# Performance work log

Hardware: AMD Instinct MI355X
Metric: run time of the kernel (lower is better)

The kernel has to match this reference:

```python
import jax, jax.numpy as jnp
import numpy as np

TEMP = 8.0      # config.router_temp
TOP_K = 2       # config.moe_top_k
EPS = 1e-8
LN_EPS = 1e-5


def _layer_norm_noaffine(x):
    # nn.LayerNorm(input_dim, elementwise_affine=False)
    mu = jnp.mean(x, axis=-1, keepdims=True)
    var = jnp.var(x, axis=-1, keepdims=True)
    return (x - mu) / jnp.sqrt(var + LN_EPS)


def _unit_norm(x):
    # x / x.norm(dim=-1).clamp(min=EPS)
    n = jnp.linalg.norm(x, axis=-1, keepdims=True)
    return x / jnp.maximum(n, EPS)


def setup_inputs() -> dict:
    key = jax.random.key(0)
    k1, k2 = jax.random.split(key)
    x = jax.random.normal(k1, (4, 4096, 2048), dtype=jnp.float32)
    prototypes = jax.random.normal(k2, (64, 2048), dtype=jnp.float32)
    return {"x": x, "prototypes": prototypes}


def reference(x, prototypes):
    # input_norm_fn = 'norm_d', proto_norm_fn = 'unit'
    xn = _layer_norm_noaffine(x)          # [b, s, d]
    pn = _unit_norm(prototypes)           # [e, d]
    logits = jnp.einsum('bsd,ed->bse', xn, pn) / TEMP   # [b, s, e]
    probs = jax.nn.softmax(logits, axis=-1)
    top_w, top_i = jax.lax.top_k(probs, TOP_K)          # [b, s, k]
    top_w = top_w / jnp.sum(top_w, axis=-1, keepdims=True)
    return top_w, top_i
```

## Files before the change

kernel.cpp:

```cpp
#include <hip/hip_runtime.h>
#include <math.h>

constexpr int kD        = 2048;
constexpr int kE        = 64;
constexpr int kWaves    = 8;
constexpr int kBlockTok = 64;
constexpr int kKpw      = kD / kWaves;
constexpr int kBK       = 16;
constexpr int kTiles    = kKpw / kBK;
constexpr int kXsStride = 20;
constexpr int kBufStride = kE + 2;

__global__ __launch_bounds__(256) void proto_prep(const float* __restrict__ p,
                                                  float* __restrict__ ws) {
  const int e   = blockIdx.x;
  const int tid = threadIdx.x;
  const float4* row = (const float4*)(p + (size_t)e * kD);
  float s = 0.f, q = 0.f;
  for (int j = tid; j < kD / 4; j += 256) {
    float4 v = row[j];
    s += (v.x + v.y) + (v.z + v.w);
    q = fmaf(v.x, v.x, fmaf(v.y, v.y, fmaf(v.z, v.z, fmaf(v.w, v.w, q))));
  }
  #pragma unroll
  for (int off = 32; off >= 1; off >>= 1) {
    s += __shfl_xor(s, off, 64);
    q += __shfl_xor(q, off, 64);
  }
  __shared__ float as[4], aq[4];
  if ((tid & 63) == 0) { as[tid >> 6] = s; aq[tid >> 6] = q; }
  __syncthreads();
  if (tid == 0) {
    float S = (as[0] + as[1]) + (as[2] + as[3]);
    float Q = (aq[0] + aq[1]) + (aq[2] + aq[3]);
    float n = fmaxf(sqrtf(Q), 1e-8f);
    ws[e]      = S;
    ws[kE + e] = 1.f / n;
  }
}

__global__ __launch_bounds__(512, 2) void router_main(
    const float* __restrict__ x, const float* __restrict__ p,
    const float* __restrict__ ws, float* __restrict__ out_w,
    float* __restrict__ out_i) {
  __shared__ float xs_all[kWaves][kBlockTok][kXsStride];
  __shared__ float buf[kBlockTok * kBufStride];
  __shared__ float sSx[kWaves][kBlockTok];
  __shared__ float sSxx[kWaves][kBlockTok];

  const int w    = threadIdx.x >> 6;
  const int lane = threadIdx.x & 63;
  const int tt   = lane & 7;
  const int te   = lane >> 3;
  const int tok0 = blockIdx.x * kBlockTok;

  const float* xw = x + (size_t)tok0 * kD + w * kKpw;
  const float* pw = p + w * kKpw;
  float* xs = &xs_all[w][0][0];

  float acc[8][8];
  #pragma unroll
  for (int i = 0; i < 8; ++i)
    #pragma unroll
    for (int j = 0; j < 8; ++j) acc[i][j] = 0.f;
  float sx = 0.f, sxx = 0.f;

  for (int kt = 0; kt < kTiles; ++kt) {
    const float* gsrc = xw + kt * kBK;
    #pragma unroll
    for (int jj = 0; jj < 4; ++jj) {
      int f = lane + 64 * jj;
      int row = f >> 2;
      int c4  = f & 3;
      float4 v = *(const float4*)(gsrc + (size_t)row * kD + c4 * 4);
      *(float4*)(xs + row * kXsStride + c4 * 4) = v;
    }
    #pragma unroll
    for (int j = 0; j < 4; ++j) {
      float4 v = *(const float4*)(xs + lane * kXsStride + j * 4);
      sx += (v.x + v.y) + (v.z + v.w);
      sxx = fmaf(v.x, v.x, fmaf(v.y, v.y, fmaf(v.z, v.z, fmaf(v.w, v.w, sxx))));
    }
    const float* pt = pw + kt * kBK;
    #pragma unroll
    for (int k4 = 0; k4 < 4; ++k4) {
      float4 pf[8];
      #pragma unroll
      for (int j = 0; j < 8; ++j)
        pf[j] = *(const float4*)(pt + (size_t)(te + 8 * j) * kD + k4 * 4);
      float4 xf[8];
      #pragma unroll
      for (int i = 0; i < 8; ++i)
        xf[i] = *(const float4*)(xs + (tt + 8 * i) * kXsStride + k4 * 4);
      #pragma unroll
      for (int i = 0; i < 8; ++i)
        #pragma unroll
        for (int j = 0; j < 8; ++j) {
          acc[i][j] = fmaf(xf[i].x, pf[j].x, acc[i][j]);
          acc[i][j] = fmaf(xf[i].y, pf[j].y, acc[i][j]);
          acc[i][j] = fmaf(xf[i].z, pf[j].z, acc[i][j]);
          acc[i][j] = fmaf(xf[i].w, pf[j].w, acc[i][j]);
        }
    }
  }

  sSx[w][lane]  = sx;
  sSxx[w][lane] = sxx;

  for (int ph = 0; ph < kWaves; ++ph) {
    __syncthreads();
    if (w == ph) {
      #pragma unroll
      for (int i = 0; i < 8; ++i)
        #pragma unroll
        for (int j = 0; j < 8; ++j) {
          float* dst = &buf[(tt + 8 * i) * kBufStride + (te + 8 * j)];
          if (ph == 0) *dst = acc[i][j];
          else         *dst += acc[i][j];
        }
    }
  }
  __syncthreads();

  const float Se  = ws[lane];
  const float inv = ws[kE + lane];
  #pragma unroll
  for (int tl = 0; tl < 8; ++tl) {
    int t = w * 8 + tl;
    float Sx = 0.f, Sq = 0.f;
    #pragma unroll
    for (int q = 0; q < kWaves; ++q) { Sx += sSx[q][t]; Sq += sSxx[q][t]; }
    float mu   = Sx * (1.f / kD);
    float var  = Sq * (1.f / kD) - mu * mu;
    float rstd = rsqrtf(var + 1e-5f);
    float Dv   = buf[t * kBufStride + lane];
    float logit = (Dv - mu * Se) * rstd * inv * 0.125f;

    float v1 = logit; int i1 = lane;
    #pragma unroll
    for (int off = 32; off >= 1; off >>= 1) {
      float ov = __shfl_xor(v1, off, 64);
      int   oi = __shfl_xor(i1, off, 64);
      if (ov > v1 || (ov == v1 && oi < i1)) { v1 = ov; i1 = oi; }
    }
    float ml = (lane == i1) ? -3.402823466e38f : logit;
    float v2 = ml; int i2 = lane;
    #pragma unroll
    for (int off = 32; off >= 1; off >>= 1) {
      float ov = __shfl_xor(v2, off, 64);
      int   oi = __shfl_xor(i2, off, 64);
      if (ov > v2 || (ov == v2 && oi < i2)) { v2 = ov; i2 = oi; }
    }
    if (lane == 0) {
      int tg = tok0 + t;
      float er = expf(v2 - v1);
      float r  = 1.f / (1.f + er);
      out_w[2 * tg]     = r;
      out_w[2 * tg + 1] = er * r;
      out_i[2 * tg]     = (float)i1;
      out_i[2 * tg + 1] = (float)i2;
    }
  }
}

extern "C" void kernel_launch(void* const* d_in, const int* in_sizes, int n_in,
                              void* d_out, int out_size, void* d_ws, size_t ws_size,
                              hipStream_t stream) {
  const float* x = (const float*)d_in[0];
  const float* p = (const float*)d_in[1];
  float* ws = (float*)d_ws;
  const int T = in_sizes[0] / kD;
  float* out_w = (float*)d_out;
  float* out_i = (float*)d_out + (size_t)T * 2;

  proto_prep<<<kE, 256, 0, stream>>>(p, ws);
  router_main<<<T / kBlockTok, 512, 0, stream>>>(x, p, ws, out_w, out_i);
}
```

Before: 256.3 us.

## Compute router GEMM with split-bf16 MFMA emulating fp32 precision

Replaces the scalar-FMA fp32 GEMM with MFMA 16x16x32 bf16 instructions, splitting each fp32 value into three bf16 parts and running six cross-term MFMAs to approximate fp32 accuracy. The block tile changes to 32 tokens with 4 waves each owning 16 experts over the full K, removing the cross-wave LDS reduction, and global loads of x are register-prefetched one tile ahead. The intent is to move the dominant compute onto matrix cores. In exchange it adds per-iteration splitting of the prototype fragments (recomputed for every block) plus LDS writes of three planes, and there is a small precision risk for top-k ties.

Result: faster. 225.5 us (-12.0%).

```diff
diff --git a/kernel.cpp b/kernel.cpp
--- a/kernel.cpp
+++ b/kernel.cpp
@@ -1,15 +1,15 @@
 #include <hip/hip_runtime.h>
 #include <math.h>
 
-constexpr int kD        = 2048;
-constexpr int kE        = 64;
-constexpr int kWaves    = 8;
-constexpr int kBlockTok = 64;
-constexpr int kKpw      = kD / kWaves;
-constexpr int kBK       = 16;
-constexpr int kTiles    = kKpw / kBK;
-constexpr int kXsStride = 20;
-constexpr int kBufStride = kE + 2;
+typedef __attribute__((ext_vector_type(8))) short short8;
+typedef __attribute__((ext_vector_type(4))) float f32x4;
+
+constexpr int kD   = 2048;
+constexpr int kE   = 64;
+constexpr int kM   = 32;
+constexpr int kBK  = 128;
+constexpr int kIt  = kD / kBK;
+constexpr int kLds = 136;
 
 __global__ __launch_bounds__(256) void proto_prep(const float* __restrict__ p,
                                                   float* __restrict__ ws) {
@@ -33,108 +33,149 @@
   if (tid == 0) {
     float S = (as[0] + as[1]) + (as[2] + as[3]);
     float Q = (aq[0] + aq[1]) + (aq[2] + aq[3]);
-    float n = fmaxf(sqrtf(Q), 1e-8f);
     ws[e]      = S;
-    ws[kE + e] = 1.f / n;
-  }
-}
-
-__global__ __launch_bounds__(512, 2) void router_main(
+    ws[kE + e] = 1.f / fmaxf(sqrtf(Q), 1e-8f);
+  }
+}
+
+__device__ __forceinline__ void split3(float v, unsigned& h, unsigned& m, unsigned& l) {
+  unsigned u = __float_as_uint(v);
+  h = u & 0xFFFF0000u;
+  float r1 = v - __uint_as_float(h);
+  m = __float_as_uint(r1) & 0xFFFF0000u;
+  float r2 = r1 - __uint_as_float(m);
+  l = __float_as_uint(r2);
+}
+
+__device__ __forceinline__ void pack2(float e0, float e1,
+                                      unsigned& dh, unsigned& dm, unsigned& dl) {
+  unsigned h0, m0, l0, h1, m1, l1;
+  split3(e0, h0, m0, l0);
+  split3(e1, h1, m1, l1);
+  dh = (h0 >> 16) | h1;
+  dm = (m0 >> 16) | m1;
+  dl = (l0 >> 16) | (l1 & 0xFFFF0000u);
+}
+
+union FragU { short8 s; unsigned u[4]; };
+
+__global__ __launch_bounds__(256, 2) void router_main(
     const float* __restrict__ x, const float* __restrict__ p,
     const float* __restrict__ ws, float* __restrict__ out_w,
     float* __restrict__ out_i) {
-  __shared__ float xs_all[kWaves][kBlockTok][kXsStride];
-  __shared__ float buf[kBlockTok * kBufStride];
-  __shared__ float sSx[kWaves][kBlockTok];
-  __shared__ float sSxx[kWaves][kBlockTok];
-
-  const int w    = threadIdx.x >> 6;
-  const int lane = threadIdx.x & 63;
-  const int tt   = lane & 7;
-  const int te   = lane >> 3;
-  const int tok0 = blockIdx.x * kBlockTok;
-
-  const float* xw = x + (size_t)tok0 * kD + w * kKpw;
-  const float* pw = p + w * kKpw;
-  float* xs = &xs_all[w][0][0];
-
-  float acc[8][8];
-  #pragma unroll
-  for (int i = 0; i < 8; ++i)
-    #pragma unroll
-    for (int j = 0; j < 8; ++j) acc[i][j] = 0.f;
-  float sx = 0.f, sxx = 0.f;
-
-  for (int kt = 0; kt < kTiles; ++kt) {
-    const float* gsrc = xw + kt * kBK;
-    #pragma unroll
-    for (int jj = 0; jj < 4; ++jj) {
-      int f = lane + 64 * jj;
-      int row = f >> 2;
-      int c4  = f & 3;
-      float4 v = *(const float4*)(gsrc + (size_t)row * kD + c4 * 4);
-      *(float4*)(xs + row * kXsStride + c4 * 4) = v;
-    }
+  __shared__ unsigned short sXh[kM * kLds];
+  __shared__ unsigned short sXm[kM * kLds];
+  __shared__ unsigned short sXl[kM * kLds];
+  __shared__ float sLogit[kM * 68];
+  __shared__ float sStats[kM][2];
+
+  const int t    = threadIdx.x;
+  const int w    = t >> 6;
+  const int lane = t & 63;
+  const int ln15 = lane & 15;
+  const int q    = lane >> 4;
+  const int tok0 = blockIdx.x * kM;
+
+  const float* xg = x + (size_t)tok0 * kD;
+  const int pe = w * 16 + ln15;
+
+  f32x4 acc[2];
+  acc[0] = (f32x4){0.f, 0.f, 0.f, 0.f};
+  acc[1] = (f32x4){0.f, 0.f, 0.f, 0.f};
+  float sx[4] = {0.f, 0.f, 0.f, 0.f}, sxx[4] = {0.f, 0.f, 0.f, 0.f};
+
+  float4 pf[4];
+  #pragma unroll
+  for (int j = 0; j < 4; ++j) {
+    int f = t + 256 * j;
+    pf[j] = *(const float4*)(xg + (size_t)(f >> 5) * kD + (f & 31) * 4);
+  }
+
+  for (int it = 0; it < kIt; ++it) {
+    __syncthreads();
     #pragma unroll
     for (int j = 0; j < 4; ++j) {
-      float4 v = *(const float4*)(xs + lane * kXsStride + j * 4);
-      sx += (v.x + v.y) + (v.z + v.w);
-      sxx = fmaf(v.x, v.x, fmaf(v.y, v.y, fmaf(v.z, v.z, fmaf(v.w, v.w, sxx))));
-    }
-    const float* pt = pw + kt * kBK;
-    #pragma unroll
-    for (int k4 = 0; k4 < 4; ++k4) {
-      float4 pf[8];
+      int f   = t + 256 * j;
+      int row = f >> 5, c4 = f & 31;
+      float4 v = pf[j];
+      sx[j] += (v.x + v.y) + (v.z + v.w);
+      sxx[j] = fmaf(v.x, v.x, fmaf(v.y, v.y, fmaf(v.z, v.z, fmaf(v.w, v.w, sxx[j]))));
+      unsigned dh0, dm0, dl0, dh1, dm1, dl1;
+      pack2(v.x, v.y, dh0, dm0, dl0);
+      pack2(v.z, v.w, dh1, dm1, dl1);
+      int off = row * kLds + c4 * 4;
+      *(uint2*)&sXh[off] = make_uint2(dh0, dh1);
+      *(uint2*)&sXm[off] = make_uint2(dm0, dm1);
+      *(uint2*)&sXl[off] = make_uint2(dl0, dl1);
+    }
+    __syncthreads();
+    if (it + 1 < kIt) {
       #pragma unroll
-      for (int j = 0; j < 8; ++j)
-        pf[j] = *(const float4*)(pt + (size_t)(te + 8 * j) * kD + k4 * 4);
-      float4 xf[8];
+      for (int j = 0; j < 4; ++j) {
+        int f = t + 256 * j;
+        pf[j] = *(const float4*)(xg + (size_t)(f >> 5) * kD + (it + 1) * kBK + (f & 31) * 4);
+      }
+    }
+    #pragma unroll
+    for (int c = 0; c < 4; ++c) {
+      const float* pb = p + (size_t)pe * kD + it * kBK + c * 32 + q * 8;
+      float4 b0 = *(const float4*)(pb);
+      float4 b1 = *(const float4*)(pb + 4);
+      FragU bh, bm, bl;
+      pack2(b0.x, b0.y, bh.u[0], bm.u[0], bl.u[0]);
+      pack2(b0.z, b0.w, bh.u[1], bm.u[1], bl.u[1]);
+      pack2(b1.x, b1.y, bh.u[2], bm.u[2], bl.u[2]);
+      pack2(b1.z, b1.w, bh.u[3], bm.u[3], bl.u[3]);
       #pragma unroll
-      for (int i = 0; i < 8; ++i)
-        xf[i] = *(const float4*)(xs + (tt + 8 * i) * kXsStride + k4 * 4);
-      #pragma unroll
-      for (int i = 0; i < 8; ++i)
-        #pragma unroll
-        for (int j = 0; j < 8; ++j) {
-          acc[i][j] = fmaf(xf[i].x, pf[j].x, acc[i][j]);
-          acc[i][j] = fmaf(xf[i].y, pf[j].y, acc[i][j]);
-          acc[i][j] = fmaf(xf[i].z, pf[j].z, acc[i][j]);
-          acc[i][j] = fmaf(xf[i].w, pf[j].w, acc[i][j]);
-        }
-    }
-  }
-
-  sSx[w][lane]  = sx;
-  sSxx[w][lane] = sxx;
-
-  for (int ph = 0; ph < kWaves; ++ph) {
-    __syncthreads();
-    if (w == ph) {
-      #pragma unroll
-      for (int i = 0; i < 8; ++i)
-        #pragma unroll
-        for (int j = 0; j < 8; ++j) {
-          float* dst = &buf[(tt + 8 * i) * kBufStride + (te + 8 * j)];
-          if (ph == 0) *dst = acc[i][j];
-          else         *dst += acc[i][j];
-        }
-    }
-  }
+      for (int m = 0; m < 2; ++m) {
+        int ro = (m * 16 + ln15) * kLds + c * 32 + q * 8;
+        short8 ah = *(const short8*)&sXh[ro];
+        short8 am = *(const short8*)&sXm[ro];
+        short8 al = *(const short8*)&sXl[ro];
+        acc[m] = __builtin_amdgcn_mfma_f32_16x16x32_bf16(ah, bh.s, acc[m], 0, 0, 0);
+        acc[m] = __builtin_amdgcn_mfma_f32_16x16x32_bf16(ah, bm.s, acc[m], 0, 0, 0);
+        acc[m] = __builtin_amdgcn_mfma_f32_16x16x32_bf16(am, bh.s, acc[m], 0, 0, 0);
+        acc[m] = __builtin_amdgcn_mfma_f32_16x16x32_bf16(am, bm.s, acc[m], 0, 0, 0);
+        acc[m] = __builtin_amdgcn_mfma_f32_16x16x32_bf16(ah, bl.s, acc[m], 0, 0, 0);
+        acc[m] = __builtin_amdgcn_mfma_f32_16x16x32_bf16(al, bh.s, acc[m], 0, 0, 0);
+      }
+    }
+  }
+
+  #pragma unroll
+  for (int j = 0; j < 4; ++j) {
+    float a = sx[j], b = sxx[j];
+    #pragma unroll
+    for (int off = 16; off >= 1; off >>= 1) {
+      a += __shfl_xor(a, off, 64);
+      b += __shfl_xor(b, off, 64);
+    }
+    if ((lane & 31) == 0) {
+      int row = (t >> 5) + 8 * j;
+      sStats[row][0] = a;
+      sStats[row][1] = b;
+    }
+  }
+
+  #pragma unroll
+  for (int m = 0; m < 2; ++m)
+    #pragma unroll
+    for (int i = 0; i < 4; ++i) {
+      int tok = m * 16 + q * 4 + i;
+      sLogit[tok * 68 + w * 16 + ln15] = acc[m][i];
+    }
   __syncthreads();
 
   const float Se  = ws[lane];
   const float inv = ws[kE + lane];
   #pragma unroll
   for (int tl = 0; tl < 8; ++tl) {
-    int t = w * 8 + tl;
-    float Sx = 0.f, Sq = 0.f;
-    #pragma unroll
-    for (int q = 0; q < kWaves; ++q) { Sx += sSx[q][t]; Sq += sSxx[q][t]; }
+    int tk = w * 8 + tl;
+    float Sx = sStats[tk][0], Sq = sStats[tk][1];
     float mu   = Sx * (1.f / kD);
     float var  = Sq * (1.f / kD) - mu * mu;
     float rstd = rsqrtf(var + 1e-5f);
-    float Dv   = buf[t * kBufStride + lane];
-    float logit = (Dv - mu * Se) * rstd * inv * 0.125f;
+    float logit = (sLogit[tk * 68 + lane] - mu * Se) * rstd * inv * 0.125f;
 
     float v1 = logit; int i1 = lane;
     #pragma unroll
@@ -152,7 +193,7 @@
       if (ov > v2 || (ov == v2 && oi < i2)) { v2 = ov; i2 = oi; }
     }
     if (lane == 0) {
-      int tg = tok0 + t;
+      int tg = tok0 + tk;
       float er = expf(v2 - v1);
       float r  = 1.f / (1.f + er);
       out_w[2 * tg]     = r;
@@ -174,5 +215,5 @@
   float* out_i = (float*)d_out + (size_t)T * 2;
 
   proto_prep<<<kE, 256, 0, stream>>>(p, ws);
-  router_main<<<T / kBlockTok, 512, 0, stream>>>(x, p, ws, out_w, out_i);
-}
+  router_main<<<T / kM, 256, 0, stream>>>(x, p, ws, out_w, out_i);
+}
```
